# Performance work log

Measured on AMD Instinct MI355X. Metric: run time of the kernel, lower is better.

The kernel has to match this reference:

```python
import jax, jax.numpy as jnp
import numpy as np

D_MODEL = 1024
NUM_HEADS = 16
HEAD_DIM = D_MODEL // NUM_HEADS
THETA = 10000.0


def _rope(x, cos, sin):
    # x: [B, H, S, hd]; cos/sin: [S, hd//2] (broadcast over B, H)
    x_even = x[..., 0::2]
    x_odd = x[..., 1::2]
    y_even = x_even * cos - x_odd * sin
    y_odd = x_even * sin + x_odd * cos
    # interleave back: stack on last dim then flatten
    y = jnp.stack((y_even, y_odd), axis=-1)
    return y.reshape(x.shape)


def setup_inputs() -> dict:
    key = jax.random.key(0)
    ks = jax.random.split(key, 5)
    B, S = 2, 2048
    x = jax.random.normal(ks[0], (B, S, D_MODEL), dtype=jnp.float32)
    scale = 1.0 / np.sqrt(D_MODEL)
    Wq = jax.random.normal(ks[1], (D_MODEL, D_MODEL), dtype=jnp.float32) * scale
    Wk = jax.random.normal(ks[2], (D_MODEL, D_MODEL), dtype=jnp.float32) * scale
    Wv = jax.random.normal(ks[3], (D_MODEL, D_MODEL), dtype=jnp.float32) * scale
    Wo = jax.random.normal(ks[4], (D_MODEL, D_MODEL), dtype=jnp.float32) * scale
    token_positions = jnp.arange(S, dtype=jnp.int64 if jax.config.jax_enable_x64 else jnp.int32)
    return {"x": x, "token_positions": token_positions, "Wq": Wq, "Wk": Wk, "Wv": Wv, "Wo": Wo}


def reference(x, token_positions, Wq, Wk, Wv, Wo):
    B, S, _ = x.shape
    # nn.Linear(d,d,bias=False): y = x @ W.T
    q = (x @ Wq.T).reshape(B, S, NUM_HEADS, HEAD_DIM).transpose(0, 2, 1, 3)
    k = (x @ Wk.T).reshape(B, S, NUM_HEADS, HEAD_DIM).transpose(0, 2, 1, 3)
    v = (x @ Wv.T).reshape(B, S, NUM_HEADS, HEAD_DIM).transpose(0, 2, 1, 3)

    # RoPE tables gathered at token_positions
    freqs = 1.0 / THETA ** (jnp.arange(0, HEAD_DIM, 2, dtype=jnp.float32) / HEAD_DIM)
    angles = token_positions.astype(jnp.float32)[:, None] * freqs[None, :]  # [S, hd//2]
    cos, sin = jnp.cos(angles), jnp.sin(angles)
    q = _rope(q, cos, sin)
    k = _rope(k, cos, sin)

    scores = jnp.einsum("bhqd,bhkd->bhqk", q, k) / np.sqrt(HEAD_DIM)
    causal = jnp.tril(jnp.ones((S, S), dtype=bool))
    scores = jnp.where(causal, scores, jnp.finfo(scores.dtype).min)
    attn = jax.nn.softmax(scores, axis=-1)
    out = jnp.einsum("bhqk,bhkd->bhqd", attn, v)  # [B,H,S,hd]
    out = out.transpose(0, 2, 1, 3).reshape(B, S, D_MODEL)
    return out @ Wo.T
```

## Files before the change

kernel.cpp:

```cpp
#include <hip/hip_runtime.h>

#define S_LEN 2048
#define NH 16
#define HD 64
#define DM 1024
#define MTOT 4096

#define QSCALE 0.18033688011112042f

typedef short bf16x8 __attribute__((ext_vector_type(8)));
typedef float f32x4 __attribute__((ext_vector_type(4)));
typedef unsigned short u16x8 __attribute__((ext_vector_type(8)));

__device__ __forceinline__ unsigned short f2bf(float f) {
  unsigned int u = __builtin_bit_cast(unsigned int, f);
  u += 0x7fffu + ((u >> 16) & 1u);
  return (unsigned short)(u >> 16);
}
__device__ __forceinline__ unsigned short f2bf_fast(float f) {
  unsigned int u = __builtin_bit_cast(unsigned int, f);
  return (unsigned short)((u + 0x8000u) >> 16);
}

__device__ __forceinline__ void async_copy16(const void* g, void* l) {
  __builtin_amdgcn_global_load_lds(
      (const __attribute__((address_space(1))) unsigned int*)g,
      (__attribute__((address_space(3))) unsigned int*)l, 16, 0, 0);
}

__global__ void cvt_bf16_kernel(const float* __restrict__ src,
                                unsigned short* __restrict__ dst, int n) {
  int i = (blockIdx.x * 256 + threadIdx.x) * 8;
  if (i >= n) return;
  const float4* s = (const float4*)(src + i);
  float4 v0 = s[0], v1 = s[1];
  u16x8 o;
  o[0] = f2bf(v0.x); o[1] = f2bf(v0.y); o[2] = f2bf(v0.z); o[3] = f2bf(v0.w);
  o[4] = f2bf(v1.x); o[5] = f2bf(v1.y); o[6] = f2bf(v1.z); o[7] = f2bf(v1.w);
  *(u16x8*)(dst + i) = o;
}

__global__ void cvt_w_kernel(const float* __restrict__ w0, const float* __restrict__ w1,
                             const float* __restrict__ w2, const float* __restrict__ w3,
                             unsigned short* __restrict__ dst) {
  int z = blockIdx.y;
  const float* src = (z == 0) ? w0 : (z == 1) ? w1 : (z == 2) ? w2 : w3;
  int i = (blockIdx.x * 256 + threadIdx.x) * 8;
  const float4* s = (const float4*)(src + i);
  float4 v0 = s[0], v1 = s[1];
  u16x8 o;
  o[0] = f2bf(v0.x); o[1] = f2bf(v0.y); o[2] = f2bf(v0.z); o[3] = f2bf(v0.w);
  o[4] = f2bf(v1.x); o[5] = f2bf(v1.y); o[6] = f2bf(v1.z); o[7] = f2bf(v1.w);
  *(u16x8*)(dst + (size_t)z * DM * DM + i) = o;
}

__global__ void sincos_tab_kernel(const int* __restrict__ pos, float2* __restrict__ tab) {
  int idx = blockIdx.x * 256 + threadIdx.x;
  int s = idx >> 5, i = idx & 31;
  float fr = expf(-(float)i * 0.28782313662425574f);
  float ang = (float)pos[s] * fr;
  float sn, cs;
  sincosf(ang, &sn, &cs);
  tab[idx] = make_float2(cs, sn);
}

__device__ __forceinline__ void gemm_core(const unsigned short* __restrict__ A,
                                          const unsigned short* __restrict__ Bt,
                                          int m0, int n0, int K,
                                          char* a_lds, char* b_lds,
                                          f32x4 (&acc)[4][4]) {
  const int tid = threadIdx.x;
  const int w = tid >> 6, l = tid & 63;
  const int wr = w >> 1, wc = w & 1;
  const int c = l & 15, g = l >> 4;

  const size_t rs = (size_t)K * 2;
  const int lr = l >> 3;
  const int jsw = ((l & 7) ^ lr) << 4;
  const char* srcA = (const char*)A + ((size_t)m0 + w * 8 + lr) * rs + jsw;
  const char* srcB = (const char*)Bt + ((size_t)n0 + w * 8 + lr) * rs + jsw;
  char* dstA = a_lds + w * 1024 + l * 16;
  char* dstB = b_lds + w * 1024 + l * 16;
  const int csw = (c & 7) << 4;

  for (int kt = 0; kt < (int)rs; kt += 128) {
#pragma unroll
    for (int i = 0; i < 4; ++i) {
      async_copy16(srcA + (size_t)i * 32 * rs + kt, dstA + i * 4096);
      async_copy16(srcB + (size_t)i * 32 * rs + kt, dstB + i * 4096);
    }
    asm volatile("s_waitcnt vmcnt(0)" ::: "memory");
    __syncthreads();
#pragma unroll
    for (int kk = 0; kk < 2; ++kk) {
      bf16x8 af[4], bfv[4];
#pragma unroll
      for (int mi = 0; mi < 4; ++mi)
        af[mi] = *(const bf16x8*)(a_lds + (wr * 64 + mi * 16 + c) * 128 + ((kk * 64 + g * 16) ^ csw));
#pragma unroll
      for (int ni = 0; ni < 4; ++ni)
        bfv[ni] = *(const bf16x8*)(b_lds + (wc * 64 + ni * 16 + c) * 128 + ((kk * 64 + g * 16) ^ csw));
#pragma unroll
      for (int mi = 0; mi < 4; ++mi)
#pragma unroll
        for (int ni = 0; ni < 4; ++ni)
          acc[mi][ni] = __builtin_amdgcn_mfma_f32_16x16x32_bf16(af[mi], bfv[ni], acc[mi][ni], 0, 0, 0);
    }
    __syncthreads();
  }
}

__global__ __launch_bounds__(256)
void gemm_qkv_kernel(const unsigned short* __restrict__ X,
                     const unsigned short* __restrict__ Wq,
                     const unsigned short* __restrict__ Wk,
                     const unsigned short* __restrict__ Wv,
                     const float2* __restrict__ tab,
                     unsigned short* __restrict__ Qb,
                     unsigned short* __restrict__ Kb,
                     unsigned short* __restrict__ Vt) {
  __shared__ char a_lds[128 * 128];
  __shared__ char b_lds[128 * 128];
  const int z = blockIdx.z;
  const unsigned short* Bt = (z == 0) ? Wq : (z == 1) ? Wk : Wv;
  const int m0 = blockIdx.x * 128, n0 = blockIdx.y * 128;

  f32x4 acc[4][4] = {};
  gemm_core(X, Bt, m0, n0, DM, a_lds, b_lds, acc);

  const int tid = threadIdx.x;
  const int w = tid >> 6, l = tid & 63;
  const int wr = w >> 1, wc = w & 1;
  const int c = l & 15, g = l >> 4;

  if (z == 2) {
#pragma unroll
    for (int mi = 0; mi < 4; ++mi)
#pragma unroll
      for (int ni = 0; ni < 4; ++ni)
#pragma unroll
        for (int r = 0; r < 4; ++r) {
          int row = m0 + wr * 64 + mi * 16 + 4 * g + r;
          int col = n0 + wc * 64 + ni * 16 + c;
          int b = row >> 11, s = row & 2047;
          int h = col >> 6, d = col & 63;
          Vt[((size_t)(b * NH + h) * HD + d) * S_LEN + s] = f2bf(acc[mi][ni][r]);
        }
  } else {
    unsigned short* QK = z ? Kb : Qb;
    const float oscale = z ? 1.0f : QSCALE;
#pragma unroll
    for (int mi = 0; mi < 4; ++mi)
#pragma unroll
      for (int ni = 0; ni < 4; ++ni) {
        int col = n0 + wc * 64 + ni * 16 + c;
        int fi = (col >> 1) & 31;
        float sgn = (col & 1) ? 1.0f : -1.0f;
#pragma unroll
        for (int r = 0; r < 4; ++r) {
          int row = m0 + wr * 64 + mi * 16 + 4 * g + r;
          int b = row >> 11, s = row & 2047;
          float v = acc[mi][ni][r];
          float p = __shfl_xor(v, 1);
          float2 csn = tab[(s << 5) | fi];
          float vr = (v * csn.x + sgn * p * csn.y) * oscale;
          int h = col >> 6, d = col & 63;
          QK[((size_t)(b * NH + h) * S_LEN + s) * HD + d] = f2bf(vr);
        }
      }
  }
}

__global__ __launch_bounds__(256)
void gemm_out_kernel(const unsigned short* __restrict__ A,
                     const unsigned short* __restrict__ Wo,
                     float* __restrict__ out) {
  __shared__ char a_lds[128 * 128];
  __shared__ char b_lds[128 * 128];
  const int m0 = blockIdx.x * 128, n0 = blockIdx.y * 128;
  f32x4 acc[4][4] = {};
  gemm_core(A, Wo, m0, n0, DM, a_lds, b_lds, acc);

  const int tid = threadIdx.x;
  const int w = tid >> 6, l = tid & 63;
  const int wr = w >> 1, wc = w & 1;
  const int c = l & 15, g = l >> 4;
#pragma unroll
  for (int mi = 0; mi < 4; ++mi)
#pragma unroll
    for (int ni = 0; ni < 4; ++ni)
#pragma unroll
      for (int r = 0; r < 4; ++r) {
        int row = m0 + wr * 64 + mi * 16 + 4 * g + r;
        int col = n0 + wc * 64 + ni * 16 + c;
        out[(size_t)row * DM + col] = acc[mi][ni][r];
      }
}

#define PART_STRIDE 4160
__global__ __launch_bounds__(256, 4)
void attn_kernel(const unsigned short* __restrict__ Q,
                 const unsigned short* __restrict__ Kb,
                 const unsigned short* __restrict__ Vt,
                 float* __restrict__ part) {
  __shared__ char kbuf[2][8192];
  __shared__ char vbuf[2][8192];
  __shared__ unsigned short p_lds[4][16 * 64];
  const int tid = threadIdx.x;
  const int w = tid >> 6, l = tid & 63;
  const int g = l >> 4, c = l & 15;

  const unsigned int id = blockIdx.x;
  const int bh = id & 31;
  const int p = (id >> 5) & 1;
  const int qblk = 31 - (id >> 6);
  const int q0 = qblk * 64;

  const size_t base = (size_t)bh * (S_LEN * HD);
  const char* Kc = (const char*)(Kb + base);
  const char* Vc = (const char*)(Vt + base);

  const int lr = l >> 3;
  const int jsw = ((l & 7) << 4) ^ (lr << 4);
  const int r0 = w * 8 + lr;
  const int r1 = (4 + w) * 8 + lr;
  const char* ksrc0 = Kc + r0 * 128 + jsw;
  const char* ksrc1 = Kc + r1 * 128 + jsw;
  const char* vsrc0 = Vc + r0 * 4096 + jsw;
  const char* vsrc1 = Vc + r1 * 4096 + jsw;

  bf16x8 qf0, qf1;
  {
    const unsigned short* qp = Q + base + (size_t)(q0 + w * 16 + c) * HD + g * 8;
    qf0 = *(const bf16x8*)qp;
    qf1 = *(const bf16x8*)(qp + 32);
  }
  f32x4 oacc[4] = {};
  float rsum[4] = {0.f, 0.f, 0.f, 0.f};
  unsigned short* pl = &p_lds[w][0];
  const int csw = (c & 7) << 4;

  auto stage = [&](int buf, int t) {
    char* kd = &kbuf[buf][w * 1024 + l * 16];
    char* vd = &vbuf[buf][w * 1024 + l * 16];
    size_t ko = (size_t)t * 8192;
    size_t vo = (size_t)t * 128;
    async_copy16(ksrc0 + ko, kd);
    async_copy16(ksrc1 + ko, kd + 4096);
    async_copy16(vsrc0 + vo, vd);
    async_copy16(vsrc1 + vo, vd + 4096);
  };

  stage(0, p);
  asm volatile("s_waitcnt vmcnt(0)" ::: "memory");
  __syncthreads();
  int cur = 0;

  for (int t = p; t <= qblk; t += 2) {
    if (t + 2 <= qblk) stage(cur ^ 1, t + 2);
    const char* kl = kbuf[cur];
    const char* vl = vbuf[cur];
    const int kv0 = t * 64;

    f32x4 sc[4] = {};
    __builtin_amdgcn_s_setprio(1);
#pragma unroll
    for (int nt = 0; nt < 4; ++nt) {
      bf16x8 k0 = *(const bf16x8*)(kl + (nt * 16 + c) * 128 + ((g * 16) ^ csw));
      bf16x8 k1 = *(const bf16x8*)(kl + (nt * 16 + c) * 128 + ((64 + g * 16) ^ csw));
      sc[nt] = __builtin_amdgcn_mfma_f32_16x16x32_bf16(qf0, k0, sc[nt], 0, 0, 0);
      sc[nt] = __builtin_amdgcn_mfma_f32_16x16x32_bf16(qf1, k1, sc[nt], 0, 0, 0);
    }
    __builtin_amdgcn_s_setprio(0);

    if (t == qblk) {
#pragma unroll
      for (int nt = 0; nt < 4; ++nt)
#pragma unroll
        for (int r = 0; r < 4; ++r) {
          int kvi = kv0 + nt * 16 + c;
          int qi = q0 + w * 16 + 4 * g + r;
          sc[nt][r] = exp2f((kvi > qi) ? -1e30f : sc[nt][r]);
        }
    } else {
#pragma unroll
      for (int nt = 0; nt < 4; ++nt)
#pragma unroll
        for (int r = 0; r < 4; ++r)
          sc[nt][r] = exp2f(sc[nt][r]);
    }
#pragma unroll
    for (int nt = 0; nt < 4; ++nt)
#pragma unroll
      for (int r = 0; r < 4; ++r) {
        float pv = sc[nt][r];
        rsum[r] += pv;
        int row = 4 * g + r, col = nt * 16 + c;
        int byte = row * 128 + ((col * 2) ^ ((row & 7) << 4));
        *(unsigned short*)((char*)pl + byte) = f2bf_fast(pv);
      }
    asm volatile("" ::: "memory");
    __builtin_amdgcn_s_setprio(1);
#pragma unroll
    for (int ks = 0; ks < 2; ++ks) {
      int pbyte = c * 128 + ((ks * 64 + g * 16) ^ csw);
      bf16x8 pf = *(const bf16x8*)((char*)pl + pbyte);
#pragma unroll
      for (int nt = 0; nt < 4; ++nt) {
        bf16x8 vf = *(const bf16x8*)(vl + (nt * 16 + c) * 128 + ((ks * 64 + g * 16) ^ csw));
        oacc[nt] = __builtin_amdgcn_mfma_f32_16x16x32_bf16(pf, vf, oacc[nt], 0, 0, 0);
      }
    }
    __builtin_amdgcn_s_setprio(0);
    asm volatile("" ::: "memory");

    asm volatile("s_waitcnt vmcnt(0)" ::: "memory");
    __syncthreads();
    cur ^= 1;
  }

#pragma unroll
  for (int r = 0; r < 4; ++r) {
    float s = rsum[r];
    s += __shfl_xor(s, 1);
    s += __shfl_xor(s, 2);
    s += __shfl_xor(s, 4);
    s += __shfl_xor(s, 8);
    rsum[r] = s;
  }
  float* pa = part + ((size_t)(bh * 32 + qblk) * 2 + p) * PART_STRIDE;
#pragma unroll
  for (int nt = 0; nt < 4; ++nt)
#pragma unroll
    for (int r = 0; r < 4; ++r) {
      int row = w * 16 + 4 * g + r;
      int col = nt * 16 + c;
      __builtin_nontemporal_store(oacc[nt][r], &pa[row * 64 + col]);
    }
  if (c == 0) {
#pragma unroll
    for (int r = 0; r < 4; ++r) {
      int row = w * 16 + 4 * g + r;
      __builtin_nontemporal_store(rsum[r], &pa[4096 + row]);
    }
  }
}

__global__ __launch_bounds__(256)
void combine_kernel(const float* __restrict__ part, unsigned short* __restrict__ Ob) {
  const int qblk = blockIdx.x & 31;
  const int bh = blockIdx.x >> 5;
  const int b = bh >> 4, h = bh & 15;
  const int tid = threadIdx.x;
  const int row = tid >> 2, colb = (tid & 3) * 16;

  const float* p0 = part + ((size_t)(bh * 32 + qblk) * 2 + 0) * PART_STRIDE;
  const float* p1 = p0 + PART_STRIDE;
  float s0 = __builtin_nontemporal_load(&p0[4096 + row]);
  float s1 = __builtin_nontemporal_load(&p1[4096 + row]);
  float inv = 1.0f / (s0 + s1);

  int token = qblk * 64 + row;
  unsigned short* dst = Ob + ((size_t)b * S_LEN + token) * DM + h * HD + colb;
  const f32x4* a0 = (const f32x4*)(p0 + row * 64 + colb);
  const f32x4* a1 = (const f32x4*)(p1 + row * 64 + colb);
  u16x8 o0, o1;
#pragma unroll
  for (int q = 0; q < 2; ++q) {
    f32x4 v0 = __builtin_nontemporal_load(&a0[2 * q]);
    f32x4 v1 = __builtin_nontemporal_load(&a1[2 * q]);
    f32x4 w0 = __builtin_nontemporal_load(&a0[2 * q + 1]);
    f32x4 w1 = __builtin_nontemporal_load(&a1[2 * q + 1]);
    u16x8& oo = q ? o1 : o0;
    oo[0] = f2bf((v0[0] + v1[0]) * inv);
    oo[1] = f2bf((v0[1] + v1[1]) * inv);
    oo[2] = f2bf((v0[2] + v1[2]) * inv);
    oo[3] = f2bf((v0[3] + v1[3]) * inv);
    oo[4] = f2bf((w0[0] + w1[0]) * inv);
    oo[5] = f2bf((w0[1] + w1[1]) * inv);
    oo[6] = f2bf((w0[2] + w1[2]) * inv);
    oo[7] = f2bf((w0[3] + w1[3]) * inv);
  }
  *(u16x8*)dst = o0;
  *(u16x8*)(dst + 8) = o1;
}

extern "C" void kernel_launch(void* const* d_in, const int* in_sizes, int n_in,
                              void* d_out, int out_size, void* d_ws, size_t ws_size,
                              hipStream_t stream) {
  const float* x = (const float*)d_in[0];
  const int* tpos = (const int*)d_in[1];
  const float* wq = (const float*)d_in[2];
  const float* wk = (const float*)d_in[3];
  const float* wv = (const float*)d_in[4];
  const float* wo = (const float*)d_in[5];
  float* out = (float*)d_out;

  char* ws = (char*)d_ws;
  unsigned short* xb = (unsigned short*)(ws);
  unsigned short* wqb = (unsigned short*)(ws + 8388608);
  unsigned short* wkb = wqb + DM * DM;
  unsigned short* wvb = wqb + 2 * DM * DM;
  unsigned short* wob = wqb + 3 * DM * DM;
  unsigned short* qb = (unsigned short*)(ws + 16777216);
  unsigned short* kb = (unsigned short*)(ws + 16777216 + 8388608);
  unsigned short* vt = (unsigned short*)(ws + 16777216 + 2 * 8388608);
  unsigned short* ab = (unsigned short*)(ws + 16777216 + 3 * 8388608);
  float2* tab = (float2*)(ws + 50331648);
  float* part = (float*)(ws + 50855936);

  cvt_bf16_kernel<<<2048, 256, 0, stream>>>(x, xb, MTOT * DM);
  cvt_w_kernel<<<dim3(512, 4), 256, 0, stream>>>(wq, wk, wv, wo, wqb);
  sincos_tab_kernel<<<256, 256, 0, stream>>>(tpos, tab);

  gemm_qkv_kernel<<<dim3(32, 8, 3), 256, 0, stream>>>(xb, wqb, wkb, wvb, tab, qb, kb, vt);
  attn_kernel<<<2048, 256, 0, stream>>>(qb, kb, vt, part);
  combine_kernel<<<1024, 256, 0, stream>>>(part, ab);
  gemm_out_kernel<<<dim3(32, 8), 256, 0, stream>>>(ab, wob, out);
}
```

Before: 134.6 us.

## Triple-buffer GEMM LDS tiles with async prefetch and MFMA priority

Rewrites the shared GEMM core used by the QKV and output projections. The old loop loaded a 64-wide K tile, waited for all loads, and computed. The new loop uses a 3-stage ring of 32-wide K tiles with partial vmcnt waits, so global-to-LDS copies overlap MFMA work. It also adds a new swizzled LDS layout, precomputed read addresses and s_setprio around the MFMA block. The costs are more LDS per block (48KB instead of 32KB), which may lower occupancy, and twice as many barrier-separated iterations.

Result: slower. 143.6 us (+6.7%).

```diff
diff --git a/kernel.cpp b/kernel.cpp
--- a/kernel.cpp
+++ b/kernel.cpp
@@ -73,40 +73,74 @@
   const int w = tid >> 6, l = tid & 63;
   const int wr = w >> 1, wc = w & 1;
   const int c = l & 15, g = l >> 4;
-
   const size_t rs = (size_t)K * 2;
-  const int lr = l >> 3;
-  const int jsw = ((l & 7) ^ lr) << 4;
-  const char* srcA = (const char*)A + ((size_t)m0 + w * 8 + lr) * rs + jsw;
-  const char* srcB = (const char*)Bt + ((size_t)n0 + w * 8 + lr) * rs + jsw;
-  char* dstA = a_lds + w * 1024 + l * 16;
-  char* dstB = b_lds + w * 1024 + l * 16;
-  const int csw = (c & 7) << 4;
-
-  for (int kt = 0; kt < (int)rs; kt += 128) {
-#pragma unroll
-    for (int i = 0; i < 4; ++i) {
-      async_copy16(srcA + (size_t)i * 32 * rs + kt, dstA + i * 4096);
-      async_copy16(srcB + (size_t)i * 32 * rs + kt, dstB + i * 4096);
-    }
-    asm volatile("s_waitcnt vmcnt(0)" ::: "memory");
-    __syncthreads();
-#pragma unroll
-    for (int kk = 0; kk < 2; ++kk) {
-      bf16x8 af[4], bfv[4];
-#pragma unroll
-      for (int mi = 0; mi < 4; ++mi)
-        af[mi] = *(const bf16x8*)(a_lds + (wr * 64 + mi * 16 + c) * 128 + ((kk * 64 + g * 16) ^ csw));
+
+  const int u = (l & 7) ^ (l >> 3);
+  const int rbl = 16 * w + 2 * (l >> 3) + (u >> 2);
+  const char* sA0 = (const char*)A + ((size_t)m0 + rbl) * rs + (u & 3) * 16;
+  const char* sA1 = sA0 + 64 * rs;
+  const char* sB0 = (const char*)Bt + ((size_t)n0 + rbl) * rs + (u & 3) * 16;
+  const char* sB1 = sB0 + 64 * rs;
+  char* dA = a_lds + w * 1024 + l * 16;
+  char* dB = b_lds + w * 1024 + l * 16;
+
+  int raddrA[4], raddrB[4];
+#pragma unroll
+  for (int mi = 0; mi < 4; ++mi) {
+    int r = wr * 64 + mi * 16 + c;
+    raddrA[mi] = (r >> 1) * 128 + (((((r & 1) << 2) + g) ^ ((r >> 1) & 7)) << 4);
+    int rb = wc * 64 + mi * 16 + c;
+    raddrB[mi] = (rb >> 1) * 128 + (((((rb & 1) << 2) + g) ^ ((rb >> 1) & 7)) << 4);
+  }
+
+  auto stage = [&](int buf, int kt) {
+    const size_t ko = (size_t)kt * 64;
+    const int off = buf * 8192;
+    async_copy16(sA0 + ko, dA + off);
+    async_copy16(sA1 + ko, dA + off + 4096);
+    async_copy16(sB0 + ko, dB + off);
+    async_copy16(sB1 + ko, dB + off + 4096);
+  };
+
+  auto compute = [&](int buf) {
+    const char* al = a_lds + buf * 8192;
+    const char* bl = b_lds + buf * 8192;
+    bf16x8 af[4], bfv[4];
+#pragma unroll
+    for (int mi = 0; mi < 4; ++mi) af[mi] = *(const bf16x8*)(al + raddrA[mi]);
+#pragma unroll
+    for (int ni = 0; ni < 4; ++ni) bfv[ni] = *(const bf16x8*)(bl + raddrB[ni]);
+    __builtin_amdgcn_s_setprio(1);
+#pragma unroll
+    for (int mi = 0; mi < 4; ++mi)
 #pragma unroll
       for (int ni = 0; ni < 4; ++ni)
-        bfv[ni] = *(const bf16x8*)(b_lds + (wc * 64 + ni * 16 + c) * 128 + ((kk * 64 + g * 16) ^ csw));
-#pragma unroll
-      for (int mi = 0; mi < 4; ++mi)
-#pragma unroll
-        for (int ni = 0; ni < 4; ++ni)
-          acc[mi][ni] = __builtin_amdgcn_mfma_f32_16x16x32_bf16(af[mi], bfv[ni], acc[mi][ni], 0, 0, 0);
-    }
-    __syncthreads();
+        acc[mi][ni] = __builtin_amdgcn_mfma_f32_16x16x32_bf16(af[mi], bfv[ni], acc[mi][ni], 0, 0, 0);
+    __builtin_amdgcn_s_setprio(0);
+  };
+
+  const int nsteps = K / 32;
+  stage(0, 0);
+  stage(1, 1);
+  stage(2, 2);
+
+  int buf = 0;
+  for (int kt = 0; kt < nsteps; ++kt) {
+    if (kt < nsteps - 2)
+      asm volatile("s_waitcnt vmcnt(8)" ::: "memory");
+    else if (kt == nsteps - 2)
+      asm volatile("s_waitcnt vmcnt(4)" ::: "memory");
+    else
+      asm volatile("s_waitcnt vmcnt(0)" ::: "memory");
+    __builtin_amdgcn_s_barrier();
+    compute(buf);
+    if (kt + 3 < nsteps) {
+      __builtin_amdgcn_s_barrier();
+      stage(buf, kt + 3);
+    } else if (kt + 1 < nsteps) {
+      __builtin_amdgcn_s_barrier();
+    }
+    buf = (buf == 2) ? 0 : buf + 1;
   }
 }
 
@@ -119,8 +153,8 @@
                      unsigned short* __restrict__ Qb,
                      unsigned short* __restrict__ Kb,
                      unsigned short* __restrict__ Vt) {
-  __shared__ char a_lds[128 * 128];
-  __shared__ char b_lds[128 * 128];
+  __shared__ char a_lds[3 * 8192];
+  __shared__ char b_lds[3 * 8192];
   const int z = blockIdx.z;
   const unsigned short* Bt = (z == 0) ? Wq : (z == 1) ? Wk : Wv;
   const int m0 = blockIdx.x * 128, n0 = blockIdx.y * 128;
@@ -175,8 +209,8 @@
 void gemm_out_kernel(const unsigned short* __restrict__ A,
                      const unsigned short* __restrict__ Wo,
                      float* __restrict__ out) {
-  __shared__ char a_lds[128 * 128];
-  __shared__ char b_lds[128 * 128];
+  __shared__ char a_lds[3 * 8192];
+  __shared__ char b_lds[3 * 8192];
   const int m0 = blockIdx.x * 128, n0 = blockIdx.y * 128;
   f32x4 acc[4][4] = {};
   gemm_core(A, Wo, m0, n0, DM, a_lds, b_lds, acc);
```
